# Optimization experiments

Hardware: AMD Instinct MI355X
Metric: run time of the kernel (lower is better)

## Reference

```python
import jax, jax.numpy as jnp
import numpy as np

INV_SQRT3 = 1.0 / np.sqrt(3.0)


def setup_inputs() -> dict:
    key = jax.random.key(0)
    ks = jax.random.split(key, 7)
    N = 100000
    M0, M1 = 128, 64  # multiplicities of 0e and 1o irreps in in1 / out
    data_in1 = jax.random.normal(ks[0], (N, M0 + 3 * M1), jnp.float32)  # [N, 320]
    data_in2 = jax.random.normal(ks[1], (N, 1 + 3), jnp.float32)        # [N, 4] = 1x0e + 1x1o
    # e3nn-style path weights, standard normal init (path_normalization='none')
    W00 = jax.random.normal(ks[2], (M0, 1, M0), jnp.float32)  # 0e x 0e -> 0e
    W01 = jax.random.normal(ks[3], (M0, 1, M1), jnp.float32)  # 0e x 1o -> 1o
    W10 = jax.random.normal(ks[4], (M1, 1, M1), jnp.float32)  # 1o x 0e -> 1o
    W11 = jax.random.normal(ks[5], (M1, 1, M0), jnp.float32)  # 1o x 1o -> 0e
    # fan_in of the scalar output slice = 128*1 (0e x 0e) + 64*1 (1o x 1o) = 192
    sqrt_k = 1.0 / np.sqrt(M0 + M1)
    bias = jax.random.uniform(ks[6], (M0,), jnp.float32, -sqrt_k, sqrt_k)
    return {"data_in1": data_in1, "data_in2": data_in2,
            "W00": W00, "W01": W01, "W10": W10, "W11": W11, "bias": bias}


def reference(data_in1, data_in2, W00, W01, W10, W11, bias):
    M0, M1 = W00.shape[0], W10.shape[0]
    N = data_in1.shape[0]
    s1 = data_in1[:, :M0]                      # [N, 128]  scalars 0e
    v1 = data_in1[:, M0:].reshape(N, M1, 3)    # [N, 64, 3] vectors 1o
    s2 = data_in2[:, :1]                       # [N, 1]    scalar attr
    v2 = data_in2[:, 1:].reshape(N, 1, 3)      # [N, 1, 3] vector attr
    # CG paths (component irrep-normalization, path_normalization='none'):
    # wigner-3j folded analytically; net per-path coefs are 1,1,1,1/sqrt(3)
    out0 = jnp.einsum('nu,nv,uvw->nw', s1, s2, W00)                       # 0e x 0e -> 0e
    out0 = out0 + INV_SQRT3 * jnp.einsum('nui,nvi,uvw->nw', v1, v2, W11)  # 1o x 1o -> 0e
    outv = jnp.einsum('nu,nvk,uvw->nwk', s1, v2, W01)                     # 0e x 1o -> 1o
    outv = outv + jnp.einsum('nuk,nv,uvw->nwk', v1, s2, W10)              # 1o x 0e -> 1o
    # indexed bias add: bias_idx selects the l=0 output slice [0:M0]
    out0 = out0 + bias
    return jnp.concatenate([out0, outv.reshape(N, M1 * 3)], axis=1)      # [N, 320]
```

## Files before the change

### kernel.cpp

```cpp
#include <hip/hip_runtime.h>

typedef __bf16 bf16_8 __attribute__((ext_vector_type(8)));
typedef float  f32x4  __attribute__((ext_vector_type(4)));

#define INV_SQRT3f 0.57735026918962576f

__global__ __launch_bounds__(256, 2) void tp_fused_kernel(
    const float* __restrict__ din1, const float* __restrict__ din2,
    const float* __restrict__ W00, const float* __restrict__ W01,
    const float* __restrict__ W10, const float* __restrict__ W11,
    const float* __restrict__ bias,
    float* __restrict__ out, int N, int npairs)
{
    __shared__ __attribute__((aligned(16))) __bf16 smem[32768];
    __bf16* sw00 = smem;
    __bf16* sw01 = smem + 16384;
    __bf16* sw11 = smem + 24576;

    const int tid = threadIdx.x;

    {
        const int c  = tid & 127, par  = tid >> 7;
        const int c2 = tid & 63,  par2 = tid >> 6;
#pragma unroll 8
        for (int i = 0; i < 64; ++i) {
            int k = par + 2 * i;
            sw00[(c * 16 + ((k >> 3) ^ (c & 15))) * 8 + (k & 7)] =
                (__bf16)W00[k * 128 + c];
        }
#pragma unroll 8
        for (int i = 0; i < 32; ++i) {
            int k = par2 + 4 * i;
            sw01[(c2 * 16 + ((k >> 3) ^ (c2 & 15))) * 8 + (k & 7)] =
                (__bf16)W01[k * 64 + c2];
        }
#pragma unroll 8
        for (int i = 0; i < 32; ++i) {
            int k = par + 2 * i;
            sw11[(c * 8 + ((k >> 3) ^ (c & 7))) * 8 + (k & 7)] =
                (__bf16)W11[k * 128 + c];
        }
    }
    __syncthreads();

    const int wid = (blockIdx.x << 2) + (tid >> 6);
    if (wid < npairs) {
        const int lane = tid & 63;
        const int mh = lane & 15;
        const int kq = lane >> 4;

        int row0 = wid * 32 + mh;       if (row0 >= N) row0 = N - 1;
        int row1 = wid * 32 + 16 + mh;  if (row1 >= N) row1 = N - 1;
        const float* __restrict__ r1a = din1 + row0 * 320;
        const float* __restrict__ r1b = din1 + row1 * 320;
        const f32x4 d2a = *(const f32x4*)(din2 + row0 * 4);
        const f32x4 d2b = *(const f32x4*)(din2 + row1 * 4);
        const float s2a = d2a.x, s2b = d2b.x;

        f32x4 accA[2][8];
        f32x4 accB[2][4];
        f32x4 accC[2][3][4];
#pragma unroll
        for (int st = 0; st < 2; ++st) {
#pragma unroll
            for (int i = 0; i < 8; ++i) accA[st][i] = (f32x4)0.0f;
#pragma unroll
            for (int i = 0; i < 4; ++i) accB[st][i] = (f32x4)0.0f;
#pragma unroll
            for (int kv = 0; kv < 3; ++kv)
#pragma unroll
                for (int i = 0; i < 4; ++i) accC[st][kv][i] = (f32x4)0.0f;
        }

#pragma unroll
        for (int s = 0; s < 4; ++s) {
            const int off = 32 * s + 8 * kq;
            f32x4 xa0 = *(const f32x4*)(r1a + off);
            f32x4 xa1 = *(const f32x4*)(r1a + off + 4);
            f32x4 xb0 = *(const f32x4*)(r1b + off);
            f32x4 xb1 = *(const f32x4*)(r1b + off + 4);
            float xxa[8] = {xa0.x, xa0.y, xa0.z, xa0.w, xa1.x, xa1.y, xa1.z, xa1.w};
            float xxb[8] = {xb0.x, xb0.y, xb0.z, xb0.w, xb1.x, xb1.y, xb1.z, xb1.w};
            bf16_8 apl_a, as2_a, apl_b, as2_b;
#pragma unroll
            for (int j = 0; j < 8; ++j) {
                apl_a[j] = (__bf16)xxa[j];
                as2_a[j] = (__bf16)(s2a * xxa[j]);
                apl_b[j] = (__bf16)xxb[j];
                as2_b[j] = (__bf16)(s2b * xxb[j]);
            }
            const int q = 4 * s + kq;
#pragma unroll
            for (int nt = 0; nt < 8; ++nt) {
                int c = nt * 16 + mh;
                bf16_8 b = *(const bf16_8*)(sw00 + (c * 16 + (q ^ mh)) * 8);
                accA[0][nt] = __builtin_amdgcn_mfma_f32_16x16x32_bf16(as2_a, b, accA[0][nt], 0, 0, 0);
                accA[1][nt] = __builtin_amdgcn_mfma_f32_16x16x32_bf16(as2_b, b, accA[1][nt], 0, 0, 0);
            }
#pragma unroll
            for (int nt = 0; nt < 4; ++nt) {
                int c = nt * 16 + mh;
                bf16_8 b = *(const bf16_8*)(sw01 + (c * 16 + (q ^ mh)) * 8);
                accB[0][nt] = __builtin_amdgcn_mfma_f32_16x16x32_bf16(apl_a, b, accB[0][nt], 0, 0, 0);
                accB[1][nt] = __builtin_amdgcn_mfma_f32_16x16x32_bf16(apl_b, b, accB[1][nt], 0, 0, 0);
            }
        }

#pragma unroll
        for (int s = 0; s < 2; ++s) {
            const int voff = 128 + 96 * s + 24 * kq;
            bf16_8 at[2], ac[2][3];
            {
                const float* p = r1a + voff;
                float b24[24];
#pragma unroll
                for (int qq = 0; qq < 6; ++qq) {
                    f32x4 t4 = *(const f32x4*)(p + 4 * qq);
                    b24[4 * qq] = t4.x; b24[4 * qq + 1] = t4.y;
                    b24[4 * qq + 2] = t4.z; b24[4 * qq + 3] = t4.w;
                }
#pragma unroll
                for (int j = 0; j < 8; ++j) {
                    float e0 = b24[3 * j], e1 = b24[3 * j + 1], e2 = b24[3 * j + 2];
                    at[0][j]    = (__bf16)(INV_SQRT3f * (e0 * d2a.y + e1 * d2a.z + e2 * d2a.w));
                    ac[0][0][j] = (__bf16)(s2a * e0);
                    ac[0][1][j] = (__bf16)(s2a * e1);
                    ac[0][2][j] = (__bf16)(s2a * e2);
                }
            }
            {
                const float* p = r1b + voff;
                float b24[24];
#pragma unroll
                for (int qq = 0; qq < 6; ++qq) {
                    f32x4 t4 = *(const f32x4*)(p + 4 * qq);
                    b24[4 * qq] = t4.x; b24[4 * qq + 1] = t4.y;
                    b24[4 * qq + 2] = t4.z; b24[4 * qq + 3] = t4.w;
                }
#pragma unroll
                for (int j = 0; j < 8; ++j) {
                    float e0 = b24[3 * j], e1 = b24[3 * j + 1], e2 = b24[3 * j + 2];
                    at[1][j]    = (__bf16)(INV_SQRT3f * (e0 * d2b.y + e1 * d2b.z + e2 * d2b.w));
                    ac[1][0][j] = (__bf16)(s2b * e0);
                    ac[1][1][j] = (__bf16)(s2b * e1);
                    ac[1][2][j] = (__bf16)(s2b * e2);
                }
            }
            const int q  = 4 * s + kq;
            const int k0 = 32 * s + 8 * kq;
#pragma unroll
            for (int nt = 0; nt < 8; ++nt) {
                int c = nt * 16 + mh;
                bf16_8 b = *(const bf16_8*)(sw11 + (c * 8 + (q ^ (mh & 7))) * 8);
                accA[0][nt] = __builtin_amdgcn_mfma_f32_16x16x32_bf16(at[0], b, accA[0][nt], 0, 0, 0);
                accA[1][nt] = __builtin_amdgcn_mfma_f32_16x16x32_bf16(at[1], b, accA[1][nt], 0, 0, 0);
            }
#pragma unroll
            for (int nt = 0; nt < 4; ++nt) {
                int c = nt * 16 + mh;
                bf16_8 b;
#pragma unroll
                for (int j = 0; j < 8; ++j)
                    b[j] = (__bf16)W10[(k0 + j) * 64 + c];
                accC[0][0][nt] = __builtin_amdgcn_mfma_f32_16x16x32_bf16(ac[0][0], b, accC[0][0][nt], 0, 0, 0);
                accC[0][1][nt] = __builtin_amdgcn_mfma_f32_16x16x32_bf16(ac[0][1], b, accC[0][1][nt], 0, 0, 0);
                accC[0][2][nt] = __builtin_amdgcn_mfma_f32_16x16x32_bf16(ac[0][2], b, accC[0][2][nt], 0, 0, 0);
                accC[1][0][nt] = __builtin_amdgcn_mfma_f32_16x16x32_bf16(ac[1][0], b, accC[1][0][nt], 0, 0, 0);
                accC[1][1][nt] = __builtin_amdgcn_mfma_f32_16x16x32_bf16(ac[1][1], b, accC[1][1][nt], 0, 0, 0);
                accC[1][2][nt] = __builtin_amdgcn_mfma_f32_16x16x32_bf16(ac[1][2], b, accC[1][2][nt], 0, 0, 0);
            }
        }

#pragma unroll
        for (int st = 0; st < 2; ++st) {
            const int rowg0 = wid * 32 + st * 16 + 4 * kq;
#pragma unroll
            for (int nt = 0; nt < 8; ++nt) {
                float bi = bias[nt * 16 + mh];
#pragma unroll
                for (int r = 0; r < 4; ++r) {
                    int rowg = rowg0 + r;
                    if (rowg < N) out[rowg * 320 + nt * 16 + mh] = accA[st][nt][r] + bi;
                }
            }
#pragma unroll
            for (int r = 0; r < 4; ++r) {
                int rowg = rowg0 + r;
                int rc = rowg < N ? rowg : N - 1;
                f32x4 e2 = *(const f32x4*)(din2 + rc * 4);
#pragma unroll
                for (int nt = 0; nt < 4; ++nt) {
                    int w = nt * 16 + mh;
                    float p2 = accB[st][nt][r];
                    if (rowg < N) {
                        int base = rowg * 320 + 128 + 3 * w;
                        out[base]     = e2.y * p2 + accC[st][0][nt][r];
                        out[base + 1] = e2.z * p2 + accC[st][1][nt][r];
                        out[base + 2] = e2.w * p2 + accC[st][2][nt][r];
                    }
                }
            }
        }
    }
}

extern "C" void kernel_launch(void* const* d_in, const int* in_sizes, int n_in,
                              void* d_out, int out_size, void* d_ws, size_t ws_size,
                              hipStream_t stream)
{
    const float* din1 = (const float*)d_in[0];
    const float* din2 = (const float*)d_in[1];
    const float* W00  = (const float*)d_in[2];
    const float* W01  = (const float*)d_in[3];
    const float* W10  = (const float*)d_in[4];
    const float* W11  = (const float*)d_in[5];
    const float* bias = (const float*)d_in[6];
    float* outp = (float*)d_out;

    int N = in_sizes[0] / 320;
    int npairs  = (N + 31) / 32;
    int nblocks = (npairs + 3) / 4;

    hipLaunchKernelGGL(tp_fused_kernel, dim3(nblocks), dim3(256), 0, stream,
                       din1, din2, W00, W01, W10, W11, bias, outp, N, npairs);
}
```

Before: 269.8 us.

## Pre-convert weights to bf16 workspace and drop per-block LDS staging

Adds a small kernel that converts all four weight matrices to bf16 in an MFMA-ready layout in global workspace, so the main kernel reads B fragments straight from global/L2 and no longer fills shared memory or calls __syncthreads in every block. The main kernel now handles one 16-row strip per wave instead of two. It folds the s1⊗v2 path into three MFMAs with v2 pre-multiplied into the A operand, which removes the separate accumulator and the epilogue combine. It also replaces the uncoalesced per-element W10 global loads and writes vector outputs as float3 stores. The cost is a second launch, weight fragments coming from global memory instead of LDS, and less B-fragment reuse per wave.

```diff
diff --git a/kernel.cpp b/kernel.cpp
--- a/kernel.cpp
+++ b/kernel.cpp
@@ -2,203 +2,165 @@
 
 typedef __bf16 bf16_8 __attribute__((ext_vector_type(8)));
 typedef float  f32x4  __attribute__((ext_vector_type(4)));
+typedef float  f32x3  __attribute__((ext_vector_type(3), aligned(4)));
 
 #define INV_SQRT3f 0.57735026918962576f
 
-__global__ __launch_bounds__(256, 2) void tp_fused_kernel(
-    const float* __restrict__ din1, const float* __restrict__ din2,
+
+__global__ void tp_convert_weights(
     const float* __restrict__ W00, const float* __restrict__ W01,
     const float* __restrict__ W10, const float* __restrict__ W11,
-    const float* __restrict__ bias,
-    float* __restrict__ out, int N, int npairs)
+    __bf16* __restrict__ ws)
 {
-    __shared__ __attribute__((aligned(16))) __bf16 smem[32768];
-    __bf16* sw00 = smem;
-    __bf16* sw01 = smem + 16384;
-    __bf16* sw11 = smem + 24576;
+    const int chunk = blockIdx.x * blockDim.x + threadIdx.x;
+    bf16_8 v;
+    if (chunk < 2048) {
+        const int c = chunk >> 4, q = chunk & 15;
+#pragma unroll
+        for (int j = 0; j < 8; ++j) v[j] = (__bf16)W00[(q * 8 + j) * 128 + c];
+        *(bf16_8*)(ws + chunk * 8) = v;
+    } else if (chunk < 3072) {
+        const int idx = chunk - 2048;
+        const int c = idx >> 4, q = idx & 15;
+#pragma unroll
+        for (int j = 0; j < 8; ++j) v[j] = (__bf16)W01[(q * 8 + j) * 64 + c];
+        *(bf16_8*)(ws + 16384 + idx * 8) = v;
+    } else if (chunk < 4096) {
+        const int idx = chunk - 3072;
+        const int c = idx >> 3, q = idx & 7;
+#pragma unroll
+        for (int j = 0; j < 8; ++j) v[j] = (__bf16)W11[(q * 8 + j) * 128 + c];
+        *(bf16_8*)(ws + 24576 + idx * 8) = v;
+    } else if (chunk < 4608) {
+        const int idx = chunk - 4096;
+        const int c = idx >> 3, q = idx & 7;
+#pragma unroll
+        for (int j = 0; j < 8; ++j) v[j] = (__bf16)W10[(q * 8 + j) * 64 + c];
+        *(bf16_8*)(ws + 32768 + idx * 8) = v;
+    }
+}
 
-    const int tid = threadIdx.x;
+__global__ __launch_bounds__(256, 2) void tp_main_kernel(
+    const float* __restrict__ din1, const float* __restrict__ din2,
+    const __bf16* __restrict__ wsw, const float* __restrict__ bias,
+    float* __restrict__ out, int N, int nstrips)
+{
+    const int tid  = threadIdx.x;
+    const int wid  = (blockIdx.x << 2) + (tid >> 6);
+    if (wid >= nstrips) return;
 
-    {
-        const int c  = tid & 127, par  = tid >> 7;
-        const int c2 = tid & 63,  par2 = tid >> 6;
-#pragma unroll 8
-        for (int i = 0; i < 64; ++i) {
-            int k = par + 2 * i;
-            sw00[(c * 16 + ((k >> 3) ^ (c & 15))) * 8 + (k & 7)] =
-                (__bf16)W00[k * 128 + c];
+    const int lane = tid & 63;
+    const int mh   = lane & 15;
+    const int kq   = lane >> 4;
+
+    int row = wid * 16 + mh;  if (row >= N) row = N - 1;
+    const float* __restrict__ r1 = din1 + row * 320;
+    const f32x4 d2 = *(const f32x4*)(din2 + row * 4);
+    const float s2 = d2.x;
+
+    const __bf16* __restrict__ w00 = wsw;
+    const __bf16* __restrict__ w01 = wsw + 16384;
+    const __bf16* __restrict__ w11 = wsw + 24576;
+    const __bf16* __restrict__ w10 = wsw + 32768;
+
+    f32x4 accA[8];
+    f32x4 accV[3][4];
+#pragma unroll
+    for (int i = 0; i < 8; ++i) accA[i] = (f32x4)0.0f;
+#pragma unroll
+    for (int k = 0; k < 3; ++k)
+#pragma unroll
+        for (int i = 0; i < 4; ++i) accV[k][i] = (f32x4)0.0f;
+
+#pragma unroll
+    for (int s = 0; s < 4; ++s) {
+        const int off = 32 * s + 8 * kq;
+        f32x4 x0 = *(const f32x4*)(r1 + off);
+        f32x4 x1 = *(const f32x4*)(r1 + off + 4);
+        float xx[8] = {x0.x, x0.y, x0.z, x0.w, x1.x, x1.y, x1.z, x1.w};
+        bf16_8 as2, av0, av1, av2;
+#pragma unroll
+        for (int j = 0; j < 8; ++j) {
+            as2[j] = (__bf16)(s2   * xx[j]);
+            av0[j] = (__bf16)(d2.y * xx[j]);
+            av1[j] = (__bf16)(d2.z * xx[j]);
+            av2[j] = (__bf16)(d2.w * xx[j]);
         }
-#pragma unroll 8
-        for (int i = 0; i < 32; ++i) {
-            int k = par2 + 4 * i;
-            sw01[(c2 * 16 + ((k >> 3) ^ (c2 & 15))) * 8 + (k & 7)] =
-                (__bf16)W01[k * 64 + c2];
+        const int q = 4 * s + kq;
+#pragma unroll
+        for (int nt = 0; nt < 8; ++nt) {
+            const int c = nt * 16 + mh;
+            bf16_8 b = *(const bf16_8*)(w00 + (c * 16 + q) * 8);
+            accA[nt] = __builtin_amdgcn_mfma_f32_16x16x32_bf16(as2, b, accA[nt], 0, 0, 0);
         }
-#pragma unroll 8
-        for (int i = 0; i < 32; ++i) {
-            int k = par + 2 * i;
-            sw11[(c * 8 + ((k >> 3) ^ (c & 7))) * 8 + (k & 7)] =
-                (__bf16)W11[k * 128 + c];
+#pragma unroll
+        for (int nt = 0; nt < 4; ++nt) {
+            const int c = nt * 16 + mh;
+            bf16_8 b = *(const bf16_8*)(w01 + (c * 16 + q) * 8);
+            accV[0][nt] = __builtin_amdgcn_mfma_f32_16x16x32_bf16(av0, b, accV[0][nt], 0, 0, 0);
+            accV[1][nt] = __builtin_amdgcn_mfma_f32_16x16x32_bf16(av1, b, accV[1][nt], 0, 0, 0);
+            accV[2][nt] = __builtin_amdgcn_mfma_f32_16x16x32_bf16(av2, b, accV[2][nt], 0, 0, 0);
         }
     }
-    __syncthreads();
-
-    const int wid = (blockIdx.x << 2) + (tid >> 6);
-    if (wid < npairs) {
-        const int lane = tid & 63;
-        const int mh = lane & 15;
-        const int kq = lane >> 4;
-
-        int row0 = wid * 32 + mh;       if (row0 >= N) row0 = N - 1;
-        int row1 = wid * 32 + 16 + mh;  if (row1 >= N) row1 = N - 1;
-        const float* __restrict__ r1a = din1 + row0 * 320;
-        const float* __restrict__ r1b = din1 + row1 * 320;
-        const f32x4 d2a = *(const f32x4*)(din2 + row0 * 4);
-        const f32x4 d2b = *(const f32x4*)(din2 + row1 * 4);
-        const float s2a = d2a.x, s2b = d2b.x;
-
-        f32x4 accA[2][8];
-        f32x4 accB[2][4];
-        f32x4 accC[2][3][4];
-#pragma unroll
-        for (int st = 0; st < 2; ++st) {
-#pragma unroll
-            for (int i = 0; i < 8; ++i) accA[st][i] = (f32x4)0.0f;
-#pragma unroll
-            for (int i = 0; i < 4; ++i) accB[st][i] = (f32x4)0.0f;
-#pragma unroll
-            for (int kv = 0; kv < 3; ++kv)
-#pragma unroll
-                for (int i = 0; i < 4; ++i) accC[st][kv][i] = (f32x4)0.0f;
-        }
 
 #pragma unroll
-        for (int s = 0; s < 4; ++s) {
-            const int off = 32 * s + 8 * kq;
-            f32x4 xa0 = *(const f32x4*)(r1a + off);
-            f32x4 xa1 = *(const f32x4*)(r1a + off + 4);
-            f32x4 xb0 = *(const f32x4*)(r1b + off);
-            f32x4 xb1 = *(const f32x4*)(r1b + off + 4);
-            float xxa[8] = {xa0.x, xa0.y, xa0.z, xa0.w, xa1.x, xa1.y, xa1.z, xa1.w};
-            float xxb[8] = {xb0.x, xb0.y, xb0.z, xb0.w, xb1.x, xb1.y, xb1.z, xb1.w};
-            bf16_8 apl_a, as2_a, apl_b, as2_b;
+    for (int s = 0; s < 2; ++s) {
+        const int voff = 128 + 96 * s + 24 * kq;
+        float b24[24];
 #pragma unroll
-            for (int j = 0; j < 8; ++j) {
-                apl_a[j] = (__bf16)xxa[j];
-                as2_a[j] = (__bf16)(s2a * xxa[j]);
-                apl_b[j] = (__bf16)xxb[j];
-                as2_b[j] = (__bf16)(s2b * xxb[j]);
-            }
-            const int q = 4 * s + kq;
+        for (int qq = 0; qq < 6; ++qq) {
+            f32x4 t4 = *(const f32x4*)(r1 + voff + 4 * qq);
+            b24[4 * qq]     = t4.x; b24[4 * qq + 1] = t4.y;
+            b24[4 * qq + 2] = t4.z; b24[4 * qq + 3] = t4.w;
+        }
+        bf16_8 at, ac0, ac1, ac2;
 #pragma unroll
-            for (int nt = 0; nt < 8; ++nt) {
-                int c = nt * 16 + mh;
-                bf16_8 b = *(const bf16_8*)(sw00 + (c * 16 + (q ^ mh)) * 8);
-                accA[0][nt] = __builtin_amdgcn_mfma_f32_16x16x32_bf16(as2_a, b, accA[0][nt], 0, 0, 0);
-                accA[1][nt] = __builtin_amdgcn_mfma_f32_16x16x32_bf16(as2_b, b, accA[1][nt], 0, 0, 0);
-            }
+        for (int j = 0; j < 8; ++j) {
+            const float e0 = b24[3 * j], e1 = b24[3 * j + 1], e2 = b24[3 * j + 2];
+            at[j]  = (__bf16)(INV_SQRT3f * (e0 * d2.y + e1 * d2.z + e2 * d2.w));
+            ac0[j] = (__bf16)(s2 * e0);
+            ac1[j] = (__bf16)(s2 * e1);
+            ac2[j] = (__bf16)(s2 * e2);
+        }
+        const int q = 4 * s + kq;
+#pragma unroll
+        for (int nt = 0; nt < 8; ++nt) {
+            const int c = nt * 16 + mh;
+            bf16_8 b = *(const bf16_8*)(w11 + (c * 8 + q) * 8);
+            accA[nt] = __builtin_amdgcn_mfma_f32_16x16x32_bf16(at, b, accA[nt], 0, 0, 0);
+        }
+#pragma unroll
+        for (int nt = 0; nt < 4; ++nt) {
+            const int c = nt * 16 + mh;
+            bf16_8 b = *(const bf16_8*)(w10 + (c * 8 + q) * 8);
+            accV[0][nt] = __builtin_amdgcn_mfma_f32_16x16x32_bf16(ac0, b, accV[0][nt], 0, 0, 0);
+            accV[1][nt] = __builtin_amdgcn_mfma_f32_16x16x32_bf16(ac1, b, accV[1][nt], 0, 0, 0);
+            accV[2][nt] = __builtin_amdgcn_mfma_f32_16x16x32_bf16(ac2, b, accV[2][nt], 0, 0, 0);
+        }
+    }
+
+    const int rowg0 = wid * 16 + 4 * kq;
+#pragma unroll
+    for (int nt = 0; nt < 8; ++nt) {
+        const float bi = bias[nt * 16 + mh];
+#pragma unroll
+        for (int r = 0; r < 4; ++r) {
+            const int rowg = rowg0 + r;
+            if (rowg < N) out[rowg * 320 + nt * 16 + mh] = accA[nt][r] + bi;
+        }
+    }
+#pragma unroll
+    for (int r = 0; r < 4; ++r) {
+        const int rowg = rowg0 + r;
+        if (rowg < N) {
 #pragma unroll
             for (int nt = 0; nt < 4; ++nt) {
-                int c = nt * 16 + mh;
-                bf16_8 b = *(const bf16_8*)(sw01 + (c * 16 + (q ^ mh)) * 8);
-                accB[0][nt] = __builtin_amdgcn_mfma_f32_16x16x32_bf16(apl_a, b, accB[0][nt], 0, 0, 0);
-                accB[1][nt] = __builtin_amdgcn_mfma_f32_16x16x32_bf16(apl_b, b, accB[1][nt], 0, 0, 0);
-            }
-        }
-
-#pragma unroll
-        for (int s = 0; s < 2; ++s) {
-            const int voff = 128 + 96 * s + 24 * kq;
-            bf16_8 at[2], ac[2][3];
-            {
-                const float* p = r1a + voff;
-                float b24[24];
-#pragma unroll
-                for (int qq = 0; qq < 6; ++qq) {
-                    f32x4 t4 = *(const f32x4*)(p + 4 * qq);
-                    b24[4 * qq] = t4.x; b24[4 * qq + 1] = t4.y;
-                    b24[4 * qq + 2] = t4.z; b24[4 * qq + 3] = t4.w;
-                }
-#pragma unroll
-                for (int j = 0; j < 8; ++j) {
-                    float e0 = b24[3 * j], e1 = b24[3 * j + 1], e2 = b24[3 * j + 2];
-                    at[0][j]    = (__bf16)(INV_SQRT3f * (e0 * d2a.y + e1 * d2a.z + e2 * d2a.w));
-                    ac[0][0][j] = (__bf16)(s2a * e0);
-                    ac[0][1][j] = (__bf16)(s2a * e1);
-                    ac[0][2][j] = (__bf16)(s2a * e2);
-                }
-            }
-            {
-                const float* p = r1b + voff;
-                float b24[24];
-#pragma unroll
-                for (int qq = 0; qq < 6; ++qq) {
-                    f32x4 t4 = *(const f32x4*)(p + 4 * qq);
-                    b24[4 * qq] = t4.x; b24[4 * qq + 1] = t4.y;
-                    b24[4 * qq + 2] = t4.z; b24[4 * qq + 3] = t4.w;
-                }
-#pragma unroll
-                for (int j = 0; j < 8; ++j) {
-                    float e0 = b24[3 * j], e1 = b24[3 * j + 1], e2 = b24[3 * j + 2];
-                    at[1][j]    = (__bf16)(INV_SQRT3f * (e0 * d2b.y + e1 * d2b.z + e2 * d2b.w));
-                    ac[1][0][j] = (__bf16)(s2b * e0);
-                    ac[1][1][j] = (__bf16)(s2b * e1);
-                    ac[1][2][j] = (__bf16)(s2b * e2);
-                }
-            }
-            const int q  = 4 * s + kq;
-            const int k0 = 32 * s + 8 * kq;
-#pragma unroll
-            for (int nt = 0; nt < 8; ++nt) {
-                int c = nt * 16 + mh;
-                bf16_8 b = *(const bf16_8*)(sw11 + (c * 8 + (q ^ (mh & 7))) * 8);
-                accA[0][nt] = __builtin_amdgcn_mfma_f32_16x16x32_bf16(at[0], b, accA[0][nt], 0, 0, 0);
-                accA[1][nt] = __builtin_amdgcn_mfma_f32_16x16x32_bf16(at[1], b, accA[1][nt], 0, 0, 0);
-            }
-#pragma unroll
-            for (int nt = 0; nt < 4; ++nt) {
-                int c = nt * 16 + mh;
-                bf16_8 b;
-#pragma unroll
-                for (int j = 0; j < 8; ++j)
-                    b[j] = (__bf16)W10[(k0 + j) * 64 + c];
-                accC[0][0][nt] = __builtin_amdgcn_mfma_f32_16x16x32_bf16(ac[0][0], b, accC[0][0][nt], 0, 0, 0);
-                accC[0][1][nt] = __builtin_amdgcn_mfma_f32_16x16x32_bf16(ac[0][1], b, accC[0][1][nt], 0, 0, 0);
-                accC[0][2][nt] = __builtin_amdgcn_mfma_f32_16x16x32_bf16(ac[0][2], b, accC[0][2][nt], 0, 0, 0);
-                accC[1][0][nt] = __builtin_amdgcn_mfma_f32_16x16x32_bf16(ac[1][0], b, accC[1][0][nt], 0, 0, 0);
-                accC[1][1][nt] = __builtin_amdgcn_mfma_f32_16x16x32_bf16(ac[1][1], b, accC[1][1][nt], 0, 0, 0);
-                accC[1][2][nt] = __builtin_amdgcn_mfma_f32_16x16x32_bf16(ac[1][2], b, accC[1][2][nt], 0, 0, 0);
-            }
-        }
-
-#pragma unroll
-        for (int st = 0; st < 2; ++st) {
-            const int rowg0 = wid * 32 + st * 16 + 4 * kq;
-#pragma unroll
-            for (int nt = 0; nt < 8; ++nt) {
-                float bi = bias[nt * 16 + mh];
-#pragma unroll
-                for (int r = 0; r < 4; ++r) {
-                    int rowg = rowg0 + r;
-                    if (rowg < N) out[rowg * 320 + nt * 16 + mh] = accA[st][nt][r] + bi;
-                }
-            }
-#pragma unroll
-            for (int r = 0; r < 4; ++r) {
-                int rowg = rowg0 + r;
-                int rc = rowg < N ? rowg : N - 1;
-                f32x4 e2 = *(const f32x4*)(din2 + rc * 4);
-#pragma unroll
-                for (int nt = 0; nt < 4; ++nt) {
-                    int w = nt * 16 + mh;
-                    float p2 = accB[st][nt][r];
-                    if (rowg < N) {
-                        int base = rowg * 320 + 128 + 3 * w;
-                        out[base]     = e2.y * p2 + accC[st][0][nt][r];
-                        out[base + 1] = e2.z * p2 + accC[st][1][nt][r];
-                        out[base + 2] = e2.w * p2 + accC[st][2][nt][r];
-                    }
-                }
+                const int w = nt * 16 + mh;
+                f32x3 o;
+                o.x = accV[0][nt][r];
+                o.y = accV[1][nt][r];
+                o.z = accV[2][nt][r];
+                *(f32x3*)(out + rowg * 320 + 128 + 3 * w) = o;
             }
         }
     }
@@ -216,11 +178,14 @@
     const float* W11  = (const float*)d_in[5];
     const float* bias = (const float*)d_in[6];
     float* outp = (float*)d_out;
+    __bf16* ws = (__bf16*)d_ws;
 
-    int N = in_sizes[0] / 320;
-    int npairs  = (N + 31) / 32;
-    int nblocks = (npairs + 3) / 4;
+    const int N = in_sizes[0] / 320;
+    const int nstrips = (N + 15) / 16;
+    const int nblocks = (nstrips + 3) / 4;
 
-    hipLaunchKernelGGL(tp_fused_kernel, dim3(nblocks), dim3(256), 0, stream,
-                       din1, din2, W00, W01, W10, W11, bias, outp, N, npairs);
+    hipLaunchKernelGGL(tp_convert_weights, dim3(18), dim3(256), 0, stream,
+                       W00, W01, W10, W11, ws);
+    hipLaunchKernelGGL(tp_main_kernel, dim3(nblocks), dim3(256), 0, stream,
+                       din1, din2, ws, bias, outp, N, nstrips);
 }
```

After: 293.1 us. 1.09x slower.
